# Optimization experiments

Measured on AMD Instinct MI355X. Metric: run time of the kernel, lower is better.

The kernel has to match this reference:

```python
import jax, jax.numpy as jnp
import numpy as np

N_NODES = 100000
N_EDGES = 1600000
IN_C, HID_C, OUT_C, K = 128, 128, 64, 3


def setup_inputs() -> dict:
    key = jax.random.key(0)
    ks = jax.random.split(key, 8)
    x = jax.random.normal(ks[0], (N_NODES, IN_C), dtype=jnp.float32)
    edge_index = jax.random.randint(ks[1], (2, N_EDGES), 0, N_NODES, dtype=jnp.int64)
    s = 0.05
    W0 = jax.random.normal(ks[2], (K, IN_C, HID_C), dtype=jnp.float32) * s
    b0 = jnp.zeros((HID_C,), dtype=jnp.float32)
    W1 = jax.random.normal(ks[3], (K, HID_C, HID_C), dtype=jnp.float32) * s
    b1 = jnp.zeros((HID_C,), dtype=jnp.float32)
    W2 = jax.random.normal(ks[4], (K, HID_C, OUT_C), dtype=jnp.float32) * s
    b2 = jnp.zeros((OUT_C,), dtype=jnp.float32)
    return {"x": x, "edge_index": edge_index, "W0": W0, "b0": b0,
            "W1": W1, "b1": b1, "W2": W2, "b2": b2}


def reference(x, edge_index, W0, b0, W1, b1, W2, b2):
    # PyG ChebConv with normalization='sym', lambda_max=2.0:
    # L_hat = L - I = -D^{-1/2} A D^{-1/2}  (self-loop weight nets to zero)
    src, dst = edge_index[0], edge_index[1]
    n = x.shape[0]
    deg = jax.ops.segment_sum(jnp.ones(src.shape, x.dtype), src, num_segments=n)
    dinv = jnp.where(deg > 0, jax.lax.rsqrt(deg), 0.0)
    w = -dinv[src] * dinv[dst]  # [E] edge weights of L_hat

    def prop(h):  # y[dst] += w * h[src]  (sparse L_hat @ h)
        return jax.ops.segment_sum(w[:, None] * h[src], dst, num_segments=n)

    def cheb_conv(h, W, b):
        # Tx_0 = h; Tx_1 = L_hat h; Tx_k = 2 L_hat Tx_{k-1} - Tx_{k-2}
        Tx0 = h
        out = Tx0 @ W[0]
        Tx1 = prop(Tx0)
        out = out + Tx1 @ W[1]
        for k in range(2, W.shape[0]):
            Tx2 = 2.0 * prop(Tx1) - Tx0
            out = out + Tx2 @ W[k]
            Tx0, Tx1 = Tx1, Tx2
        return out + b

    h = jax.nn.relu(cheb_conv(x, W0, b0))   # dropout is identity in eval mode
    h = jax.nn.relu(cheb_conv(h, W1, b1))
    return cheb_conv(h, W2, b2)
```

## Files before the change

### kernel.cpp

```cpp
#include <hip/hip_runtime.h>
#include <hip/hip_bf16.h>

#define NN 100000
#define NE 1600000
#define NB 196
#define BSH 9
#define SCH 4096

typedef __attribute__((ext_vector_type(8))) short short8;
typedef __attribute__((ext_vector_type(4))) float f32x4;

__device__ __forceinline__ unsigned bf16r(float x) {
    unsigned u = __float_as_uint(x);
    return (u + 0x7fffu + ((u >> 16) & 1u)) >> 16;
}
__device__ __forceinline__ unsigned pack_bf16(float a, float b) {
    return bf16r(a) | (bf16r(b) << 16);
}
__device__ __forceinline__ void unpack2(int b, float& lo, float& hi) {
    lo = __uint_as_float(((unsigned)b) << 16);
    hi = __uint_as_float(((unsigned)b) & 0xffff0000u);
}

__global__ __launch_bounds__(256) void hist_kernel(const int* __restrict__ src,
                                                   const int* __restrict__ dst,
                                                   int* __restrict__ binS,
                                                   int* __restrict__ binD, int E) {
    __shared__ int hS[NB], hD[NB];
    for (int i = threadIdx.x; i < NB; i += 256) { hS[i] = 0; hD[i] = 0; }
    __syncthreads();
    for (int e = blockIdx.x * 256 + threadIdx.x; e < E; e += gridDim.x * 256) {
        atomicAdd(&hS[src[e] >> BSH], 1);
        atomicAdd(&hD[dst[e] >> BSH], 1);
    }
    __syncthreads();
    for (int i = threadIdx.x; i < NB; i += 256) {
        if (hS[i]) atomicAdd(&binS[i], hS[i]);
        if (hD[i]) atomicAdd(&binD[i], hD[i]);
    }
}

__global__ void scan_kernel(const int* __restrict__ binS, const int* __restrict__ binD,
                            int* __restrict__ curS, int* __restrict__ offS,
                            int* __restrict__ curD, int* __restrict__ offD,
                            int* __restrict__ rowptr, int E) {
    if (threadIdx.x == 0 && blockIdx.x == 0) {
        int rs = 0, rd = 0;
        for (int i = 0; i < NB; ++i) {
            curS[i] = rs; offS[i] = rs; rs += binS[i];
            curD[i] = rd; offD[i] = rd; rd += binD[i];
        }
        offS[NB] = rs;
        offD[NB] = rd;
        rowptr[NN] = E;
    }
}

__global__ __launch_bounds__(256) void scatter_kernel(const int* __restrict__ src,
                                                      const int* __restrict__ dst,
                                                      int* __restrict__ curS,
                                                      int* __restrict__ curD,
                                                      int* __restrict__ srcB,
                                                      int* __restrict__ packB, int E) {
    __shared__ int cS[NB], cD[NB], bS[NB], bD[NB];
    int base = blockIdx.x * SCH;
    for (int i = threadIdx.x; i < NB; i += 256) { cS[i] = 0; cD[i] = 0; }
    __syncthreads();
    int s[16], d[16], rS[16], rD[16];
#pragma unroll
    for (int k = 0; k < 16; ++k) {
        int idx = base + k * 256 + threadIdx.x;
        if (idx < E) {
            s[k] = src[idx]; d[k] = dst[idx];
            rS[k] = atomicAdd(&cS[s[k] >> BSH], 1);
            rD[k] = atomicAdd(&cD[d[k] >> BSH], 1);
        } else {
            s[k] = -1;
        }
    }
    __syncthreads();
    for (int i = threadIdx.x; i < NB; i += 256) {
        if (cS[i]) bS[i] = atomicAdd(&curS[i], cS[i]);
        if (cD[i]) bD[i] = atomicAdd(&curD[i], cD[i]);
    }
    __syncthreads();
#pragma unroll
    for (int k = 0; k < 16; ++k) {
        if (s[k] >= 0) {
            srcB[bS[s[k] >> BSH] + rS[k]] = s[k];
            packB[bD[d[k] >> BSH] + rD[k]] = s[k] | ((d[k] & 511) << 20);
        }
    }
}

__global__ __launch_bounds__(256) void csr_kernel(const int* __restrict__ offD,
                                                  const int* __restrict__ packB,
                                                  int* __restrict__ rowptr,
                                                  int* __restrict__ csrCol, int n) {
    int b = blockIdx.x;
    int node0 = b << BSH;
    int nNodes = min(512, n - node0);
    if (nNodes <= 0) return;
    int beg = offD[b], end = offD[b + 1];
    __shared__ int h[512];
    __shared__ int roff[512];
    for (int i = threadIdx.x; i < 512; i += 256) h[i] = 0;
    __syncthreads();
    for (int p = beg + threadIdx.x; p < end; p += 256)
        atomicAdd(&h[(packB[p] >> 20) & 511], 1);
    __syncthreads();
    if (threadIdx.x == 0) {
        int r = beg;
        for (int i = 0; i < 512; ++i) { roff[i] = r; r += h[i]; }
    }
    __syncthreads();
    for (int i = threadIdx.x; i < nNodes; i += 256) rowptr[node0 + i] = roff[i];
    for (int i = threadIdx.x; i < 512; i += 256) h[i] = 0;
    __syncthreads();
    for (int p = beg + threadIdx.x; p < end; p += 256) {
        int pk = packB[p];
        int dl = (pk >> 20) & 511;
        int r = atomicAdd(&h[dl], 1);
        csrCol[roff[dl] + r] = pk & 0xFFFFF;
    }
}

__global__ __launch_bounds__(256) void deg_kernel(const int* __restrict__ offS,
                                                  const int* __restrict__ srcB,
                                                  float* __restrict__ dinv, int n) {
    int b = blockIdx.x;
    int node0 = b << BSH;
    int nNodes = min(512, n - node0);
    if (nNodes <= 0) return;
    int beg = offS[b], end = offS[b + 1];
    __shared__ int h[512];
    for (int i = threadIdx.x; i < 512; i += 256) h[i] = 0;
    __syncthreads();
    for (int p = beg + threadIdx.x; p < end; p += 256)
        atomicAdd(&h[srcB[p] & 511], 1);
    __syncthreads();
    for (int i = threadIdx.x; i < nNodes; i += 256) {
        int d = h[i];
        dinv[node0 + i] = d > 0 ? rsqrtf((float)d) : 0.0f;
    }
}

__global__ void convw_kernel(const float* __restrict__ W0, const float* __restrict__ W1,
                             const float* __restrict__ W2, short* __restrict__ Bt0,
                             short* __restrict__ Bt1, short* __restrict__ Bt2) {
    int i = blockIdx.x * blockDim.x + threadIdx.x;
    if (i < 49152) {
        int j = i >> 7, k = i & 127;
        int t = j >> 7, o = j & 127;
        float v = (t == 0) ? W0[k * 128 + o] - W0[2 * 16384 + k * 128 + o]
                : (t == 1) ? W0[16384 + k * 128 + o]
                           : 2.f * W0[2 * 16384 + k * 128 + o];
        Bt0[j * 128 + k] = (short)bf16r(v);
    } else if (i < 98304) {
        int m = i - 49152;
        int j = m >> 7, k = m & 127;
        int t = j >> 7, o = j & 127;
        float v = (t == 0) ? W1[k * 128 + o] - W1[2 * 16384 + k * 128 + o]
                : (t == 1) ? W1[16384 + k * 128 + o]
                           : 2.f * W1[2 * 16384 + k * 128 + o];
        Bt1[j * 128 + k] = (short)bf16r(v);
    } else if (i < 122880) {
        int m = i - 98304;
        int j = m >> 7, k = m & 127;
        int t = j >> 6, o = j & 63;
        float v = (t == 0) ? W2[k * 64 + o] - W2[2 * 8192 + k * 64 + o]
                : (t == 1) ? W2[8192 + k * 64 + o]
                           : 2.f * W2[2 * 8192 + k * 64 + o];
        Bt2[j * 128 + k] = (short)bf16r(v);
    }
}

template <int C, int AF32>
__global__ __launch_bounds__(512) void gemm_kernel(const void* Asrc,
                                                   const short* __restrict__ Bt,
                                                   const float* __restrict__ bias,
                                                   short* out0, short* out1, short* out2,
                                                   int n) {
    constexpr int BNT = 3 * C;
    constexpr int WC = BNT / 96;
    constexpr int WR = 8 / WC;
    constexpr int WM = 128 / WR;
    constexpr int MF = WM / 16;
    constexpr int NF = 6;
    constexpr int LDP = 40;
    __shared__ short As[128 * LDP];
    __shared__ short Bs[BNT * LDP];

    int tid = threadIdx.x;
    int lane = tid & 63;
    int wid = tid >> 6;
    int wy = wid / WC;
    int wx = wid % WC;
    int row0 = blockIdx.x * 128;
    int l15 = lane & 15;
    int kb = (lane >> 4) * 8;

    f32x4 acc[MF][NF];
#pragma unroll
    for (int i = 0; i < MF; ++i)
#pragma unroll
        for (int j = 0; j < NF; ++j) acc[i][j] = (f32x4){0.f, 0.f, 0.f, 0.f};

    for (int k0 = 0; k0 < 128; k0 += 32) {
        {
            int r = tid >> 2, seg = tid & 3;
            int gr = row0 + r;
            short8 v = (short8){0, 0, 0, 0, 0, 0, 0, 0};
            if (gr < n) {
                if (AF32) {
                    const float* xp = (const float*)Asrc + (size_t)gr * 128 + k0 + seg * 8;
                    float4 f0 = *(const float4*)xp;
                    float4 f1 = *(const float4*)(xp + 4);
                    v[0] = (short)bf16r(f0.x); v[1] = (short)bf16r(f0.y);
                    v[2] = (short)bf16r(f0.z); v[3] = (short)bf16r(f0.w);
                    v[4] = (short)bf16r(f1.x); v[5] = (short)bf16r(f1.y);
                    v[6] = (short)bf16r(f1.z); v[7] = (short)bf16r(f1.w);
                } else {
                    v = *(const short8*)((const short*)Asrc + (size_t)gr * 128 + k0 + seg * 8);
                }
            }
            *(short8*)&As[r * LDP + seg * 8] = v;
        }
        constexpr int BSLOT = BNT * 4;
#pragma unroll
        for (int i = 0; i < (BSLOT + 511) / 512; ++i) {
            int slot = tid + i * 512;
            if (BSLOT % 512 == 0 || slot < BSLOT) {
                int j = slot >> 2, seg = slot & 3;
                *(short8*)&Bs[j * LDP + seg * 8] =
                    *(const short8*)(Bt + (size_t)j * 128 + k0 + seg * 8);
            }
        }
        __syncthreads();

        short8 af[MF], bfr[NF];
#pragma unroll
        for (int mf = 0; mf < MF; ++mf)
            af[mf] = *(short8*)&As[(wy * WM + mf * 16 + l15) * LDP + kb];
#pragma unroll
        for (int nf = 0; nf < NF; ++nf)
            bfr[nf] = *(short8*)&Bs[(wx * 96 + nf * 16 + l15) * LDP + kb];
#pragma unroll
        for (int mf = 0; mf < MF; ++mf)
#pragma unroll
            for (int nf = 0; nf < NF; ++nf)
                acc[mf][nf] = __builtin_amdgcn_mfma_f32_16x16x32_bf16(
                    af[mf], bfr[nf], acc[mf][nf], 0, 0, 0);
        __syncthreads();
    }

#pragma unroll
    for (int nf = 0; nf < NF; ++nf) {
        int colc = wx * 96 + nf * 16 + l15;
        int t = colc / C;
        int off = colc % C;
        short* P = (t == 0) ? out0 : (t == 1) ? out1 : out2;
        float bb = (t == 0) ? bias[off] : 0.f;
#pragma unroll
        for (int mf = 0; mf < MF; ++mf) {
#pragma unroll
            for (int r = 0; r < 4; ++r) {
                int row = row0 + wy * WM + mf * 16 + (lane >> 4) * 4 + r;
                if (row >= n) continue;
                P[(size_t)row * C + off] = (short)bf16r(acc[mf][nf][r] + bb);
            }
        }
    }
}

template <int C, int RELU, int OUTF>
__global__ __launch_bounds__(256) void prop_kernel(const short* __restrict__ G,
                                                   const short* __restrict__ Add,
                                                   void* __restrict__ O,
                                                   const int* __restrict__ rowptr,
                                                   const int* __restrict__ csrCol,
                                                   const float* __restrict__ dinv, int n) {
    constexpr int LPE = C / 8;
    constexpr int EPG = 64 / LPE;
    constexpr int STEP = 4 * EPG;
    int wid = (blockIdx.x * blockDim.x + threadIdx.x) >> 6;
    int lane = threadIdx.x & 63;
    if (wid >= n) return;
    int beg = rowptr[wid];
    int c = rowptr[wid + 1] - beg;
    int sg = lane / LPE;
    int sl = lane & (LPE - 1);
    float a0 = 0, a1 = 0, a2 = 0, a3 = 0, a4 = 0, a5 = 0, a6 = 0, a7 = 0;
    for (int b0 = 0; b0 < c; b0 += 64) {
        int cb = min(64, c - b0);
        int myc = 0; float mydv = 0.f;
        if (lane < cb) {
            myc = csrCol[beg + b0 + lane];
            mydv = dinv[myc];
        }
        for (int base = 0; base < cb; base += STEP) {
            int j0 = base + sg, j1 = j0 + EPG, j2 = j0 + 2 * EPG, j3 = j0 + 3 * EPG;
            int   s0 = __shfl(myc, j0);  float w0 = __shfl(mydv, j0);
            int   s1 = __shfl(myc, j1);  float w1 = __shfl(mydv, j1);
            int   s2 = __shfl(myc, j2);  float w2 = __shfl(mydv, j2);
            int   s3 = __shfl(myc, j3);  float w3 = __shfl(mydv, j3);
            int4 v0 = *(const int4*)(G + (size_t)s0 * C + sl * 8);
            int4 v1 = *(const int4*)(G + (size_t)s1 * C + sl * 8);
            int4 v2 = *(const int4*)(G + (size_t)s2 * C + sl * 8);
            int4 v3 = *(const int4*)(G + (size_t)s3 * C + sl * 8);
            float lo, hi;
            unpack2(v0.x, lo, hi); a0 = fmaf(w0, lo, a0); a1 = fmaf(w0, hi, a1);
            unpack2(v0.y, lo, hi); a2 = fmaf(w0, lo, a2); a3 = fmaf(w0, hi, a3);
            unpack2(v0.z, lo, hi); a4 = fmaf(w0, lo, a4); a5 = fmaf(w0, hi, a5);
            unpack2(v0.w, lo, hi); a6 = fmaf(w0, lo, a6); a7 = fmaf(w0, hi, a7);
            unpack2(v1.x, lo, hi); a0 = fmaf(w1, lo, a0); a1 = fmaf(w1, hi, a1);
            unpack2(v1.y, lo, hi); a2 = fmaf(w1, lo, a2); a3 = fmaf(w1, hi, a3);
            unpack2(v1.z, lo, hi); a4 = fmaf(w1, lo, a4); a5 = fmaf(w1, hi, a5);
            unpack2(v1.w, lo, hi); a6 = fmaf(w1, lo, a6); a7 = fmaf(w1, hi, a7);
            unpack2(v2.x, lo, hi); a0 = fmaf(w2, lo, a0); a1 = fmaf(w2, hi, a1);
            unpack2(v2.y, lo, hi); a2 = fmaf(w2, lo, a2); a3 = fmaf(w2, hi, a3);
            unpack2(v2.z, lo, hi); a4 = fmaf(w2, lo, a4); a5 = fmaf(w2, hi, a5);
            unpack2(v2.w, lo, hi); a6 = fmaf(w2, lo, a6); a7 = fmaf(w2, hi, a7);
            unpack2(v3.x, lo, hi); a0 = fmaf(w3, lo, a0); a1 = fmaf(w3, hi, a1);
            unpack2(v3.y, lo, hi); a2 = fmaf(w3, lo, a2); a3 = fmaf(w3, hi, a3);
            unpack2(v3.z, lo, hi); a4 = fmaf(w3, lo, a4); a5 = fmaf(w3, hi, a5);
            unpack2(v3.w, lo, hi); a6 = fmaf(w3, lo, a6); a7 = fmaf(w3, hi, a7);
        }
    }
#pragma unroll
    for (int off = LPE; off < 64; off <<= 1) {
        a0 += __shfl_xor(a0, off); a1 += __shfl_xor(a1, off);
        a2 += __shfl_xor(a2, off); a3 += __shfl_xor(a3, off);
        a4 += __shfl_xor(a4, off); a5 += __shfl_xor(a5, off);
        a6 += __shfl_xor(a6, off); a7 += __shfl_xor(a7, off);
    }
    if (lane < LPE) {
        float scale = -dinv[wid];
        int4 ad = *(const int4*)(Add + (size_t)wid * C + sl * 8);
        float r0, r1, r2, r3, r4, r5, r6, r7, lo, hi;
        unpack2(ad.x, lo, hi); r0 = fmaf(scale, a0, lo); r1 = fmaf(scale, a1, hi);
        unpack2(ad.y, lo, hi); r2 = fmaf(scale, a2, lo); r3 = fmaf(scale, a3, hi);
        unpack2(ad.z, lo, hi); r4 = fmaf(scale, a4, lo); r5 = fmaf(scale, a5, hi);
        unpack2(ad.w, lo, hi); r6 = fmaf(scale, a6, lo); r7 = fmaf(scale, a7, hi);
        if (RELU) {
            r0 = fmaxf(r0, 0.f); r1 = fmaxf(r1, 0.f); r2 = fmaxf(r2, 0.f);
            r3 = fmaxf(r3, 0.f); r4 = fmaxf(r4, 0.f); r5 = fmaxf(r5, 0.f);
            r6 = fmaxf(r6, 0.f); r7 = fmaxf(r7, 0.f);
        }
        if (OUTF) {
            float* op = (float*)O + (size_t)wid * C + sl * 8;
            *(float4*)op = make_float4(r0, r1, r2, r3);
            *(float4*)(op + 4) = make_float4(r4, r5, r6, r7);
        } else {
            int4 w;
            w.x = pack_bf16(r0, r1);
            w.y = pack_bf16(r2, r3);
            w.z = pack_bf16(r4, r5);
            w.w = pack_bf16(r6, r7);
            *(int4*)((short*)O + (size_t)wid * C + sl * 8) = w;
        }
    }
}

extern "C" void kernel_launch(void* const* d_in, const int* in_sizes, int n_in,
                              void* d_out, int out_size, void* d_ws, size_t ws_size,
                              hipStream_t stream) {
    const float* x  = (const float*)d_in[0];
    const int*   ei = (const int*)d_in[1];
    const float* W0 = (const float*)d_in[2];
    const float* b0 = (const float*)d_in[3];
    const float* W1 = (const float*)d_in[4];
    const float* b1 = (const float*)d_in[5];
    const float* W2 = (const float*)d_in[6];
    const float* b2 = (const float*)d_in[7];
    float* out = (float*)d_out;

    const int n = NN, E = NE;
    const int* src = ei;
    const int* dst = ei + E;

    char* ws = (char*)d_ws;
    auto alloc = [&](size_t bytes) -> void* {
        void* p = (void*)ws;
        ws += (bytes + 255) & ~(size_t)255;
        return p;
    };
    int*   binS   = (int*)alloc(NB * 4);
    int*   binD   = (int*)alloc(NB * 4);
    int*   curS   = (int*)alloc((NB + 1) * 4);
    int*   offS   = (int*)alloc((NB + 1) * 4);
    int*   curD   = (int*)alloc((NB + 1) * 4);
    int*   offD   = (int*)alloc((NB + 1) * 4);
    int*   srcB   = (int*)alloc((size_t)E * 4);
    int*   packB  = (int*)alloc((size_t)E * 4);
    int*   rowptr = (int*)alloc((size_t)(n + 1) * 4);
    int*   csrCol = (int*)alloc((size_t)E * 4);
    float* dinv   = (float*)alloc((size_t)n * 4);
    short* buf0   = (short*)alloc((size_t)n * 128 * 2);
    short* buf1   = (short*)alloc((size_t)n * 128 * 2);
    short* buf2   = (short*)alloc((size_t)n * 128 * 2);
    short* buf3   = (short*)alloc((size_t)n * 128 * 2);
    short* Bt0    = (short*)alloc((size_t)384 * 128 * 2);
    short* Bt1    = (short*)alloc((size_t)384 * 128 * 2);
    short* Bt2    = (short*)alloc((size_t)192 * 128 * 2);

    hipMemsetAsync(binS, 0, NB * 4, stream);
    hipMemsetAsync(binD, 0, NB * 4, stream);

    const int TPB = 256;

    hist_kernel<<<256, TPB, 0, stream>>>(src, dst, binS, binD, E);
    scan_kernel<<<1, 64, 0, stream>>>(binS, binD, curS, offS, curD, offD, rowptr, E);
    int sChunks = (E + SCH - 1) / SCH;
    scatter_kernel<<<sChunks, TPB, 0, stream>>>(src, dst, curS, curD, srcB, packB, E);
    csr_kernel<<<NB, TPB, 0, stream>>>(offD, packB, rowptr, csrCol, n);
    deg_kernel<<<NB, TPB, 0, stream>>>(offS, srcB, dinv, n);

    convw_kernel<<<(122880 + 255) / 256, 256, 0, stream>>>(W0, W1, W2, Bt0, Bt1, Bt2);

    int pBlocks = (n + 3) / 4;
    int gBlocks = (n + 127) / 128;

    gemm_kernel<128, 1><<<gBlocks, 512, 0, stream>>>(x, Bt0, b0, buf0, buf1, buf2, n);
    prop_kernel<128, 0, 0><<<pBlocks, 256, 0, stream>>>(buf2, buf1, buf3, rowptr, csrCol, dinv, n);
    prop_kernel<128, 1, 0><<<pBlocks, 256, 0, stream>>>(buf3, buf0, buf1, rowptr, csrCol, dinv, n);
    gemm_kernel<128, 0><<<gBlocks, 512, 0, stream>>>(buf1, Bt1, b1, buf0, buf1, buf2, n);
    prop_kernel<128, 0, 0><<<pBlocks, 256, 0, stream>>>(buf2, buf1, buf3, rowptr, csrCol, dinv, n);
    prop_kernel<128, 1, 0><<<pBlocks, 256, 0, stream>>>(buf3, buf0, buf1, rowptr, csrCol, dinv, n);
    gemm_kernel<64, 0><<<gBlocks, 512, 0, stream>>>(buf1, Bt2, b2, buf0, buf3, buf2, n);
    prop_kernel<64, 0, 0><<<pBlocks, 256, 0, stream>>>(buf2, buf3, buf0 + (size_t)n * 64,
                                                       rowptr, csrCol, dinv, n);
    prop_kernel<64, 0, 1><<<pBlocks, 256, 0, stream>>>(buf0 + (size_t)n * 64, buf0, out,
                                                       rowptr, csrCol, dinv, n);
}
```

Measured before the change: 592.3 us.

## Prefetch next GEMM k-tile into registers and stage epilogue through LDS

The GEMM main loop now loads the next 32-wide k-slice of A and B into registers right after the barrier, so global loads overlap the MFMA work on the current slice. The epilogue writes each warp's 16x96 output fragment into reused shared memory and then stores full 16-byte vectors to global memory instead of scattered 2-byte stores. This targets global load latency and uncoalesced output writes, at the cost of more registers and extra LDS traffic.

```diff
diff --git a/kernel.cpp b/kernel.cpp
--- a/kernel.cpp
+++ b/kernel.cpp
@@ -188,8 +188,11 @@
     constexpr int MF = WM / 16;
     constexpr int NF = 6;
     constexpr int LDP = 40;
-    __shared__ short As[128 * LDP];
-    __shared__ short Bs[BNT * LDP];
+    constexpr int BSLOT = BNT * 4;
+    constexpr int BITER = (BSLOT + 511) / 512;
+    __shared__ short lds[(128 + BNT) * LDP];
+    short* As = lds;
+    short* Bs = lds + 128 * LDP;
 
     int tid = threadIdx.x;
     int lane = tid & 63;
@@ -200,44 +203,74 @@
     int l15 = lane & 15;
     int kb = (lane >> 4) * 8;
 
+    int ar = tid >> 2, aseg = tid & 3;
+    int agr = row0 + ar;
+
     f32x4 acc[MF][NF];
 #pragma unroll
     for (int i = 0; i < MF; ++i)
 #pragma unroll
         for (int j = 0; j < NF; ++j) acc[i][j] = (f32x4){0.f, 0.f, 0.f, 0.f};
 
-    for (int k0 = 0; k0 < 128; k0 += 32) {
-        {
-            int r = tid >> 2, seg = tid & 3;
-            int gr = row0 + r;
-            short8 v = (short8){0, 0, 0, 0, 0, 0, 0, 0};
-            if (gr < n) {
-                if (AF32) {
-                    const float* xp = (const float*)Asrc + (size_t)gr * 128 + k0 + seg * 8;
-                    float4 f0 = *(const float4*)xp;
-                    float4 f1 = *(const float4*)(xp + 4);
-                    v[0] = (short)bf16r(f0.x); v[1] = (short)bf16r(f0.y);
-                    v[2] = (short)bf16r(f0.z); v[3] = (short)bf16r(f0.w);
-                    v[4] = (short)bf16r(f1.x); v[5] = (short)bf16r(f1.y);
-                    v[6] = (short)bf16r(f1.z); v[7] = (short)bf16r(f1.w);
-                } else {
-                    v = *(const short8*)((const short*)Asrc + (size_t)gr * 128 + k0 + seg * 8);
-                }
+    float4 fa0, fa1;
+    short8 va;
+    short8 vb[BITER];
+
+    auto loadA = [&](int k0) {
+        if (AF32) {
+            if (agr < n) {
+                const float* xp = (const float*)Asrc + (size_t)agr * 128 + k0 + aseg * 8;
+                fa0 = *(const float4*)xp;
+                fa1 = *(const float4*)(xp + 4);
+            } else {
+                fa0 = make_float4(0.f, 0.f, 0.f, 0.f);
+                fa1 = fa0;
             }
-            *(short8*)&As[r * LDP + seg * 8] = v;
-        }
-        constexpr int BSLOT = BNT * 4;
-#pragma unroll
-        for (int i = 0; i < (BSLOT + 511) / 512; ++i) {
+        } else {
+            va = (agr < n) ? *(const short8*)((const short*)Asrc + (size_t)agr * 128 + k0 + aseg * 8)
+                           : (short8){0, 0, 0, 0, 0, 0, 0, 0};
+        }
+    };
+    auto loadB = [&](int k0) {
+#pragma unroll
+        for (int i = 0; i < BITER; ++i) {
             int slot = tid + i * 512;
             if (BSLOT % 512 == 0 || slot < BSLOT) {
                 int j = slot >> 2, seg = slot & 3;
-                *(short8*)&Bs[j * LDP + seg * 8] =
-                    *(const short8*)(Bt + (size_t)j * 128 + k0 + seg * 8);
+                vb[i] = *(const short8*)(Bt + (size_t)j * 128 + k0 + seg * 8);
             }
         }
+    };
+
+    loadA(0);
+    loadB(0);
+
+    for (int step = 0; step < 4; ++step) {
+        {
+            short8 w;
+            if (AF32) {
+                w[0] = (short)bf16r(fa0.x); w[1] = (short)bf16r(fa0.y);
+                w[2] = (short)bf16r(fa0.z); w[3] = (short)bf16r(fa0.w);
+                w[4] = (short)bf16r(fa1.x); w[5] = (short)bf16r(fa1.y);
+                w[6] = (short)bf16r(fa1.z); w[7] = (short)bf16r(fa1.w);
+            } else {
+                w = va;
+            }
+            *(short8*)&As[ar * LDP + aseg * 8] = w;
+        }
+#pragma unroll
+        for (int i = 0; i < BITER; ++i) {
+            int slot = tid + i * 512;
+            if (BSLOT % 512 == 0 || slot < BSLOT) {
+                int j = slot >> 2, seg = slot & 3;
+                *(short8*)&Bs[j * LDP + seg * 8] = vb[i];
+            }
+        }
         __syncthreads();
-
+        if (step < 3) {
+            loadA((step + 1) * 32);
+            loadB((step + 1) * 32);
+        }
         short8 af[MF], bfr[NF];
 #pragma unroll
         for (int mf = 0; mf < MF; ++mf)
@@ -254,21 +287,34 @@
         __syncthreads();
     }
 
+    float bb[NF];
 #pragma unroll
     for (int nf = 0; nf < NF; ++nf) {
         int colc = wx * 96 + nf * 16 + l15;
-        int t = colc / C;
-        int off = colc % C;
-        short* P = (t == 0) ? out0 : (t == 1) ? out1 : out2;
-        float bb = (t == 0) ? bias[off] : 0.f;
-#pragma unroll
-        for (int mf = 0; mf < MF; ++mf) {
+        bb[nf] = (colc < C) ? bias[colc] : 0.f;
+    }
+    short* st = lds + wid * 1536;
+#pragma unroll
+    for (int mf = 0; mf < MF; ++mf) {
+#pragma unroll
+        for (int nf = 0; nf < NF; ++nf) {
 #pragma unroll
             for (int r = 0; r < 4; ++r) {
-                int row = row0 + wy * WM + mf * 16 + (lane >> 4) * 4 + r;
-                if (row >= n) continue;
-                P[(size_t)row * C + off] = (short)bf16r(acc[mf][nf][r] + bb);
+                int fr = (lane >> 4) * 4 + r;
+                st[fr * 96 + nf * 16 + l15] = (short)bf16r(acc[mf][nf][r] + bb[nf]);
             }
+        }
+#pragma unroll
+        for (int u = 0; u < 3; ++u) {
+            int unit = u * 64 + lane;
+            int rr = unit / 12;
+            int seg = unit - rr * 12;
+            int grow = row0 + wy * WM + mf * 16 + rr;
+            int colc = wx * 96 + seg * 8;
+            int t = colc / C, off = colc - t * C;
+            short* P = (t == 0) ? out0 : (t == 1) ? out1 : out2;
+            if (grow < n)
+                *(int4*)&P[(size_t)grow * C + off] = *(const int4*)&st[rr * 96 + seg * 8];
         }
     }
 }
```

New measurement: 516.0 us. -12.9%, faster.
